# Performance work log

Hardware: AMD Instinct MI355X
Metric: run time of the kernel (lower is better)

The kernel has to match this reference:

```python
import jax, jax.numpy as jnp
import numpy as np

B, S, D, H = 2, 2048, 1024, 16  # batch, seq, embed_dim, num_heads
DH = D // H                      # head dim = 64


def setup_inputs() -> dict:
    key = jax.random.key(0)
    kx, kq, kbq, kk, kbk, kv, kbv = jax.random.split(key, 7)
    scale = 1.0 / np.sqrt(D)
    return {
        "x": jax.random.normal(kx, (B, S, D), dtype=jnp.float32),
        "Wq": jax.random.normal(kq, (D, D), dtype=jnp.float32) * scale,
        "bq": jax.random.normal(kbq, (D,), dtype=jnp.float32) * 0.01,
        "Wk": jax.random.normal(kk, (D, D), dtype=jnp.float32) * scale,
        "bk": jax.random.normal(kbk, (D,), dtype=jnp.float32) * 0.01,
        "Wv": jax.random.normal(kv, (D, D), dtype=jnp.float32) * scale,
        "bv": jax.random.normal(kbv, (D,), dtype=jnp.float32) * 0.01,
    }


def reference(x, Wq, bq, Wk, bk, Wv, bv):
    # ooqkv_type == 'q', odeint_method == 'id': q branch = act(Linear(x)), exact GELU (torch nn.GELU default)
    q = jax.nn.gelu(x @ Wq + bq, approximate=False)
    k = x @ Wk + bk
    v = x @ Wv + bv
    # [B, S, D] -> [B, S, H, DH]
    q = q.reshape(B, S, H, DH)
    k = k.reshape(B, S, H, DH)
    v = v.reshape(B, S, H, DH)
    # NOTE: original module has NO 1/sqrt(d) scale — faithful reproduction
    att = jnp.einsum("bqhd,bkhd->bhqk", q, k)
    att = jax.nn.softmax(att, axis=-1)
    out = jnp.einsum("bhqk,bkhd->bqhd", att, v)
    return out.reshape(B, S, D)
```

## Files before the change

### kernel.cpp

```cpp
#include <hip/hip_runtime.h>
#include <math.h>

#define B_  2
#define S_  2048
#define D_  1024
#define H_  16
#define DH_ 64
#define M_  (B_ * S_)

typedef _Float16 half_t;
typedef __attribute__((ext_vector_type(8))) _Float16 h8;
typedef __attribute__((ext_vector_type(4))) _Float16 h4;
typedef __attribute__((ext_vector_type(4))) float   f32x4;

#define LOG2E 1.44269504088896f

__device__ __forceinline__ void gll16(const half_t* g, half_t* l) {
    __builtin_amdgcn_global_load_lds(
        (__attribute__((address_space(1))) const void*)g,
        (__attribute__((address_space(3))) void*)l, 16, 0, 0);
}

__global__ __launch_bounds__(256) void prep_k(
    const float* __restrict__ x, half_t* __restrict__ xh,
    const float* __restrict__ Wq, const float* __restrict__ Wk,
    const float* __restrict__ Wv, half_t* __restrict__ Wt)
{
    const int bx = blockIdx.x;
    if (bx < 2048) {
        const size_t i = ((size_t)bx * 256 + threadIdx.x) * 8;
        const float4 a = *(const float4*)(x + i);
        const float4 b = *(const float4*)(x + i + 4);
        h8 o;
        o[0] = (half_t)a.x; o[1] = (half_t)a.y; o[2] = (half_t)a.z; o[3] = (half_t)a.w;
        o[4] = (half_t)b.x; o[5] = (half_t)b.y; o[6] = (half_t)b.z; o[7] = (half_t)b.w;
        *(h8*)(xh + i) = o;
    } else {
        const int gb    = bx - 2048;
        const int which = gb >> 9;
        const float* __restrict__ W = (which == 0) ? Wq : (which == 1) ? Wk : Wv;
        half_t* __restrict__ T = Wt + (size_t)which * D_ * D_;
        const int gw   = (gb & 511) * 4 + (threadIdx.x >> 6);
        const int lane = threadIdx.x & 63;
        const int n    = (gw & 15) * 64 + lane;
        const int k0   = (gw >> 4) * 8;
        h8 o;
        #pragma unroll
        for (int t = 0; t < 8; ++t) o[t] = (half_t)W[(size_t)(k0 + t) * D_ + n];
        *(h8*)(T + (size_t)n * D_ + k0) = o;
    }
}

__global__ __launch_bounds__(512) void qkv_gemm_f16(
    const half_t* __restrict__ xh, const half_t* __restrict__ Wt,
    const float* __restrict__ bq, const float* __restrict__ bk,
    const float* __restrict__ bv,
    half_t* __restrict__ Qo, half_t* __restrict__ Ko, half_t* __restrict__ Vt)
{
    const int lin = blockIdx.y * 24 + blockIdx.x;
    const int xcd = lin & 7;
    const int idx = lin >> 3;
    const int n0g = (xcd * 3 + idx % 3) * 128;
    const int m0  = (idx / 3) * 128;
    const int which = n0g >> 10;
    const int n0    = n0g & 1023;
    const half_t* __restrict__ Wp  = Wt + (size_t)which * D_ * D_;
    const float* __restrict__ bias = (which == 0) ? bq : (which == 1) ? bk : bv;

    const int tid = threadIdx.x, lane = tid & 63, wave = tid >> 6;
    const int wm = (wave & 3) * 32, wn = (wave >> 2) * 64;
    const int ln = lane & 15, quad = lane >> 4;

    __shared__ __align__(16) half_t SMEM[128 * 136];
    half_t* const As = SMEM;
    half_t* const Bs = SMEM + 128 * 64;

    const int r0  = tid >> 3, c0 = tid & 7;
    const int cs  = c0 ^ (r0 & 7);
    const half_t* aS = xh + (size_t)(m0 + r0) * D_ + cs * 8;
    const half_t* bS = Wp + (size_t)(n0 + r0) * D_ + cs * 8;

    f32x4 acc[2][4];
    #pragma unroll
    for (int i = 0; i < 2; ++i)
        #pragma unroll
        for (int j = 0; j < 4; ++j) acc[i][j] = (f32x4){0.f, 0.f, 0.f, 0.f};

    for (int k0 = 0; k0 < D_; k0 += 64) {
        __syncthreads();
        gll16(aS,            &As[tid * 8]);
        gll16(aS + 64 * D_,  &As[(tid + 512) * 8]);
        gll16(bS,            &Bs[tid * 8]);
        gll16(bS + 64 * D_,  &Bs[(tid + 512) * 8]);
        aS += 64; bS += 64;
        __syncthreads();

        #pragma unroll
        for (int kc = 0; kc < 2; ++kc) {
            h8 af[2], bf[4];
            #pragma unroll
            for (int i = 0; i < 2; ++i) {
                const int r = wm + i * 16 + ln;
                af[i] = *(const h8*)&As[r * 64 + (((kc << 2) + quad) ^ (r & 7)) * 8];
            }
            #pragma unroll
            for (int j = 0; j < 4; ++j) {
                const int r = wn + j * 16 + ln;
                bf[j] = *(const h8*)&Bs[r * 64 + (((kc << 2) + quad) ^ (r & 7)) * 8];
            }
            #pragma unroll
            for (int i = 0; i < 2; ++i)
                #pragma unroll
                for (int j = 0; j < 4; ++j)
                    acc[i][j] = __builtin_amdgcn_mfma_f32_16x16x32_f16(
                        af[i], bf[j], acc[i][j], 0, 0, 0);
        }
    }

    if (which == 2) {
        #pragma unroll
        for (int j = 0; j < 4; ++j) {
            const int col = n0 + wn + j * 16 + ln;
            const int h = col >> 6, d = col & 63;
            const float bb = bias[col];
            #pragma unroll
            for (int i = 0; i < 2; ++i) {
                const int sg = m0 + wm + i * 16 + quad * 4;
                const int b  = sg >> 11, srow = sg & 2047;
                h4 pv;
                #pragma unroll
                for (int r = 0; r < 4; ++r) pv[r] = (half_t)(acc[i][j][r] + bb);
                *(h4*)(Vt + (((size_t)(b * H_ + h) * DH_ + d) * S_ + srow)) = pv;
            }
        }
    } else {
        half_t* __restrict__ outp = (which == 0) ? Qo : Ko;
        __syncthreads();
        #pragma unroll
        for (int j = 0; j < 4; ++j) {
            const int col = wn + j * 16 + ln;
            const float bb = bias[n0 + col];
            #pragma unroll
            for (int i = 0; i < 2; ++i) {
                #pragma unroll
                for (int r = 0; r < 4; ++r) {
                    const int row = wm + i * 16 + quad * 4 + r;
                    float t = acc[i][j][r] + bb;
                    if (which == 0) {
                        const float u = t * fmaf(t * t, 0.0356774081f, 0.7978845608f);
                        const float e = __builtin_amdgcn_exp2f(u * -2.88539008178f);
                        t = t * __builtin_amdgcn_rcpf(1.0f + e) * LOG2E;
                    }
                    SMEM[row * 136 + col] = (half_t)t;
                }
            }
        }
        __syncthreads();
        const int cc = tid & 15;
        const int rr = tid >> 4;
        #pragma unroll
        for (int p = 0; p < 4; ++p) {
            const int row = p * 32 + rr;
            const h8 v = *(const h8*)&SMEM[row * 136 + cc * 8];
            *(h8*)(outp + (size_t)(m0 + row) * D_ + n0 + cc * 8) = v;
        }
    }
}

#define DEFER_THR 10.0f
#define ATTN_TILE(KS, VS)                                                     \
    do {                                                                      \
        f32x4 sa[4];                                                          \
        __builtin_amdgcn_s_setprio(1);                                        \
        _Pragma("unroll")                                                     \
        for (int j = 0; j < 4; ++j) {                                         \
            const int rK = j * 16 + ln;                                       \
            const h8 ka0 = *(const h8*)&KS[rK * 64 + ((quad)     ^ (rK & 7)) * 8]; \
            const h8 ka1 = *(const h8*)&KS[rK * 64 + ((quad + 4) ^ (rK & 7)) * 8]; \
            f32x4 t = (f32x4){0.f, 0.f, 0.f, 0.f};                            \
            t = __builtin_amdgcn_mfma_f32_16x16x32_f16(ka0, qa0, t, 0, 0, 0); \
            t = __builtin_amdgcn_mfma_f32_16x16x32_f16(ka1, qa1, t, 0, 0, 0); \
            sa[j] = t;                                                        \
        }                                                                     \
        __builtin_amdgcn_s_setprio(0);                                        \
        float mxa = sa[0][0];                                                 \
        _Pragma("unroll")                                                     \
        for (int j = 0; j < 4; ++j)                                           \
            _Pragma("unroll")                                                 \
            for (int r = 0; r < 4; ++r) mxa = fmaxf(mxa, sa[j][r]);           \
        mxa = fmaxf(mxa, __shfl_xor(mxa, 16, 64));                            \
        mxa = fmaxf(mxa, __shfl_xor(mxa, 32, 64));                            \
        if (__ballot(mxa > m_a + DEFER_THR)) {                                \
            const float mna = fmaxf(m_a, mxa);                                \
            const float ala = __builtin_amdgcn_exp2f(m_a - mna);              \
            m_a = mna;                                                        \
            float ra[4];                                                      \
            _Pragma("unroll")                                                 \
            for (int r = 0; r < 4; ++r) ra[r] = __shfl(ala, quad * 4 + r, 64);\
            _Pragma("unroll")                                                 \
            for (int r = 0; r < 4; ++r) {                                     \
                la[r] *= ra[r];                                               \
                _Pragma("unroll")                                             \
                for (int j = 0; j < 4; ++j) Oa[j][r] *= ra[r];                \
            }                                                                 \
        }                                                                     \
        _Pragma("unroll")                                                     \
        for (int j = 0; j < 4; ++j) {                                         \
            h4 pva;                                                           \
            _Pragma("unroll")                                                 \
            for (int r = 0; r < 4; ++r)                                       \
                pva[r] = (half_t)__builtin_amdgcn_exp2f(sa[j][r] - m_a);      \
            *(h4*)&QPs[wave * 16 + ln][j * 16 + quad * 4] = pva;              \
        }                                                                     \
        const h8 pa0 = *(const h8*)&QPs[wave * 16 + ln][quad * 8];            \
        const h8 pa1 = *(const h8*)&QPs[wave * 16 + ln][32 + quad * 8];       \
        __builtin_amdgcn_s_setprio(1);                                        \
        _Pragma("unroll")                                                     \
        for (int j = 0; j < 4; ++j) {                                         \
            const int rV = j * 16 + ln;                                       \
            const h8 vb0 = *(const h8*)&VS[rV * 64 + ((quad)     ^ (rV & 7)) * 8]; \
            const h8 vb1 = *(const h8*)&VS[rV * 64 + ((quad + 4) ^ (rV & 7)) * 8]; \
            Oa[j] = __builtin_amdgcn_mfma_f32_16x16x32_f16(pa0, vb0, Oa[j], 0, 0, 0); \
            Oa[j] = __builtin_amdgcn_mfma_f32_16x16x32_f16(pa1, vb1, Oa[j], 0, 0, 0); \
        }                                                                     \
        la = __builtin_amdgcn_mfma_f32_16x16x32_f16(pa0, ones8, la, 0, 0, 0); \
        la = __builtin_amdgcn_mfma_f32_16x16x32_f16(pa1, ones8, la, 0, 0, 0); \
        __builtin_amdgcn_s_setprio(0);                                        \
    } while (0)

__global__ __launch_bounds__(512) void attn_f16(
    const half_t* __restrict__ Q, const half_t* __restrict__ K,
    const half_t* __restrict__ Vt, float* __restrict__ out)
{
    const int tid  = threadIdx.x;
    const int lane = tid & 63;
    const int wave = tid >> 6;
    const int ln   = lane & 15;
    const int quad = lane >> 4;

    const int lin = blockIdx.y * 16 + blockIdx.x;
    const int swz = (lin & 7) * 64 + (lin >> 3);
    const int bh  = swz >> 4;
    const int b   = bh >> 4;
    const int h   = bh & 15;
    const int q0  = (swz & 15) * 128;

    const half_t* __restrict__ Qb  = Q  + (size_t)b * S_ * D_ + h * DH_;
    const half_t* __restrict__ Kb  = K  + (size_t)b * S_ * D_ + h * DH_;
    const half_t* __restrict__ Vtb = Vt + (size_t)bh * DH_ * S_;

    __shared__ __align__(16) half_t Ks0[64 * 64];
    __shared__ __align__(16) half_t Vs0[64 * 64];
    __shared__ __align__(16) half_t Ks1[64 * 64];
    __shared__ __align__(16) half_t Vs1[64 * 64];
    __shared__ __align__(16) half_t QPs[128][72];

    const int sr  = tid >> 3, sc0 = tid & 7;
    const int scs = sc0 ^ (sr & 7);
    const half_t* kS = Kb  + (size_t)sr * D_ + scs * 8;
    const half_t* vS = Vtb + (size_t)sr * S_ + scs * 8;
    half_t* const kD0 = &Ks0[tid * 8];
    half_t* const vD0 = &Vs0[tid * 8];
    half_t* const kD1 = &Ks1[tid * 8];
    half_t* const vD1 = &Vs1[tid * 8];

    gll16(kS, kD0); gll16(vS, vD0);
    kS += 64 * D_; vS += 64;

    #pragma unroll
    for (int l = 0; l < 2; ++l) {
        const int c = tid + l * 512;
        const int r = c >> 3, k8 = c & 7;
        *(h8*)&QPs[r][k8 * 8] = *(const h8*)(Qb + (size_t)(q0 + r) * D_ + k8 * 8);
    }
    __syncthreads();
    const h8 qa0 = *(const h8*)&QPs[wave * 16 + ln][quad * 8];
    const h8 qa1 = *(const h8*)&QPs[wave * 16 + ln][32 + quad * 8];

    h8 ones8;
    #pragma unroll
    for (int t = 0; t < 8; ++t) ones8[t] = (half_t)1.0f;

    f32x4 Oa[4];
    #pragma unroll
    for (int j = 0; j < 4; ++j) Oa[j] = (f32x4){0.f, 0.f, 0.f, 0.f};
    f32x4 la = (f32x4){0.f, 0.f, 0.f, 0.f};
    float m_a = -INFINITY;

    for (int it = 0; it < 16; ++it) {
        gll16(kS, kD1); gll16(vS, vD1);
        kS += 64 * D_; vS += 64;
        ATTN_TILE(Ks0, Vs0);
        __syncthreads();

        if (it < 15) {
            gll16(kS, kD0); gll16(vS, vD0);
            kS += 64 * D_; vS += 64;
        }
        ATTN_TILE(Ks1, Vs1);
        __syncthreads();
    }

    #pragma unroll
    for (int r = 0; r < 4; ++r) {
        const float iva = 1.0f / la[r];
        const int rowa = q0 + wave * 16 + quad * 4 + r;
        #pragma unroll
        for (int j = 0; j < 4; ++j)
            out[((size_t)b * S_ + rowa) * D_ + h * DH_ + j * 16 + ln] = Oa[j][r] * iva;
    }
}

extern "C" void kernel_launch(void* const* d_in, const int* in_sizes, int n_in,
                              void* d_out, int out_size, void* d_ws, size_t ws_size,
                              hipStream_t stream) {
    const float* x  = (const float*)d_in[0];
    const float* Wq = (const float*)d_in[1];
    const float* bq = (const float*)d_in[2];
    const float* Wk = (const float*)d_in[3];
    const float* bk = (const float*)d_in[4];
    const float* Wv = (const float*)d_in[5];
    const float* bv = (const float*)d_in[6];
    float* out = (float*)d_out;

    const size_t nmd = (size_t)M_ * D_;
    const size_t ndd = (size_t)D_ * D_;
    half_t* xh  = (half_t*)d_ws;
    half_t* Wt  = xh + nmd;
    half_t* Qh  = Wt + 3 * ndd;
    half_t* Kh  = Qh + nmd;
    half_t* Vtw = Kh + nmd;

    prep_k<<<2048 + 1536, 256, 0, stream>>>(x, xh, Wq, Wk, Wv, Wt);
    qkv_gemm_f16<<<dim3(3 * D_ / 128, M_ / 128), 512, 0, stream>>>(
        xh, Wt, bq, bk, bv, Qh, Kh, Vtw);
    attn_f16<<<dim3(S_ / 128, B_ * H_), 512, 0, stream>>>(Qh, Kh, Vtw, out);
}
```

Before: 168.3 us.

## Double-buffer QKV GEMM LDS tiles with BK=32 and tree-reduce attention row max

```diff
diff --git a/kernel.cpp b/kernel.cpp
--- a/kernel.cpp
+++ b/kernel.cpp
@@ -51,6 +51,32 @@
     }
 }
 
+#define QSLOT(r, q) \
+    (((((r) >> 1) * 8) + ((((((r) & 1) << 2) | (q))) ^ (((r) >> 1) & 7))) * 8)
+
+#define QKV_STEP(AS, BS)                                                      \
+    do {                                                                      \
+        h8 af[2], bf[4];                                                      \
+        _Pragma("unroll")                                                     \
+        for (int i = 0; i < 2; ++i) {                                         \
+            const int r = wm + i * 16 + ln;                                   \
+            af[i] = *(const h8*)&AS[QSLOT(r, quad)];                          \
+        }                                                                     \
+        _Pragma("unroll")                                                     \
+        for (int j = 0; j < 4; ++j) {                                         \
+            const int r = wn + j * 16 + ln;                                   \
+            bf[j] = *(const h8*)&BS[QSLOT(r, quad)];                          \
+        }                                                                     \
+        __builtin_amdgcn_s_setprio(1);                                        \
+        _Pragma("unroll")                                                     \
+        for (int i = 0; i < 2; ++i)                                           \
+            _Pragma("unroll")                                                 \
+            for (int j = 0; j < 4; ++j)                                       \
+                acc[i][j] = __builtin_amdgcn_mfma_f32_16x16x32_f16(           \
+                    af[i], bf[j], acc[i][j], 0, 0, 0);                        \
+        __builtin_amdgcn_s_setprio(0);                                        \
+    } while (0)
+
 __global__ __launch_bounds__(512) void qkv_gemm_f16(
     const half_t* __restrict__ xh, const half_t* __restrict__ Wt,
     const float* __restrict__ bq, const float* __restrict__ bk,
@@ -71,14 +97,17 @@
     const int wm = (wave & 3) * 32, wn = (wave >> 2) * 64;
     const int ln = lane & 15, quad = lane >> 4;
 
-    __shared__ __align__(16) half_t SMEM[128 * 136];
-    half_t* const As = SMEM;
-    half_t* const Bs = SMEM + 128 * 64;
-
-    const int r0  = tid >> 3, c0 = tid & 7;
-    const int cs  = c0 ^ (r0 & 7);
-    const half_t* aS = xh + (size_t)(m0 + r0) * D_ + cs * 8;
-    const half_t* bS = Wp + (size_t)(n0 + r0) * D_ + cs * 8;
+    __shared__ __align__(16) half_t As0[128 * 40];
+    __shared__ __align__(16) half_t Bs0[128 * 40];
+    __shared__ __align__(16) half_t As1[128 * 40];
+    __shared__ __align__(16) half_t Bs1[128 * 40];
+
+    const int srow = tid >> 3, sch = tid & 7;
+    const int v    = sch ^ (srow & 7);
+    const int sr   = srow * 2 + (v >> 2);
+    const int sk   = (v & 3) * 8;
+    const half_t* aS = xh + (size_t)(m0 + sr) * D_ + sk;
+    const half_t* bS = Wp + (size_t)(n0 + sr) * D_ + sk;
 
     f32x4 acc[2][4];
     #pragma unroll
@@ -86,35 +115,25 @@
         #pragma unroll
         for (int j = 0; j < 4; ++j) acc[i][j] = (f32x4){0.f, 0.f, 0.f, 0.f};
 
-    for (int k0 = 0; k0 < D_; k0 += 64) {
-        __syncthreads();
-        gll16(aS,            &As[tid * 8]);
-        gll16(aS + 64 * D_,  &As[(tid + 512) * 8]);
-        gll16(bS,            &Bs[tid * 8]);
-        gll16(bS + 64 * D_,  &Bs[(tid + 512) * 8]);
-        aS += 64; bS += 64;
-        __syncthreads();
-
-        #pragma unroll
-        for (int kc = 0; kc < 2; ++kc) {
-            h8 af[2], bf[4];
-            #pragma unroll
-            for (int i = 0; i < 2; ++i) {
-                const int r = wm + i * 16 + ln;
-                af[i] = *(const h8*)&As[r * 64 + (((kc << 2) + quad) ^ (r & 7)) * 8];
-            }
-            #pragma unroll
-            for (int j = 0; j < 4; ++j) {
-                const int r = wn + j * 16 + ln;
-                bf[j] = *(const h8*)&Bs[r * 64 + (((kc << 2) + quad) ^ (r & 7)) * 8];
-            }
-            #pragma unroll
-            for (int i = 0; i < 2; ++i)
-                #pragma unroll
-                for (int j = 0; j < 4; ++j)
-                    acc[i][j] = __builtin_amdgcn_mfma_f32_16x16x32_f16(
-                        af[i], bf[j], acc[i][j], 0, 0, 0);
-        }
+    gll16(aS, &As0[tid * 8]);
+    gll16(bS, &Bs0[tid * 8]);
+    aS += 32; bS += 32;
+    __syncthreads();
+
+    for (int it = 0; it < 16; ++it) {
+        gll16(aS, &As1[tid * 8]);
+        gll16(bS, &Bs1[tid * 8]);
+        aS += 32; bS += 32;
+        QKV_STEP(As0, Bs0);
+        __syncthreads();
+
+        if (it < 15) {
+            gll16(aS, &As0[tid * 8]);
+            gll16(bS, &Bs0[tid * 8]);
+            aS += 32; bS += 32;
+        }
+        QKV_STEP(As1, Bs1);
+        __syncthreads();
     }
 
     if (which == 2) {
@@ -126,20 +145,22 @@
             #pragma unroll
             for (int i = 0; i < 2; ++i) {
                 const int sg = m0 + wm + i * 16 + quad * 4;
-                const int b  = sg >> 11, srow = sg & 2047;
+                const int b  = sg >> 11, srw = sg & 2047;
                 h4 pv;
                 #pragma unroll
                 for (int r = 0; r < 4; ++r) pv[r] = (half_t)(acc[i][j][r] + bb);
-                *(h4*)(Vt + (((size_t)(b * H_ + h) * DH_ + d) * S_ + srow)) = pv;
+                *(h4*)(Vt + (((size_t)(b * H_ + h) * DH_ + d) * S_ + srw)) = pv;
             }
         }
     } else {
         half_t* __restrict__ outp = (which == 0) ? Qo : Ko;
-        __syncthreads();
         #pragma unroll
         for (int j = 0; j < 4; ++j) {
             const int col = wn + j * 16 + ln;
             const float bb = bias[n0 + col];
+            half_t* const pb = (wave & 4) ? ((j & 2) ? Bs1 : As1)
+                                          : ((j & 2) ? Bs0 : As0);
+            const int c32 = (j & 1) * 16 + ln;
             #pragma unroll
             for (int i = 0; i < 2; ++i) {
                 #pragma unroll
@@ -151,18 +172,21 @@
                         const float e = __builtin_amdgcn_exp2f(u * -2.88539008178f);
                         t = t * __builtin_amdgcn_rcpf(1.0f + e) * LOG2E;
                     }
-                    SMEM[row * 136 + col] = (half_t)t;
+                    pb[row * 40 + c32] = (half_t)t;
                 }
             }
         }
         __syncthreads();
         const int cc = tid & 15;
         const int rr = tid >> 4;
+        half_t* const pb = (cc & 8) ? ((cc & 4) ? Bs1 : As1)
+                                    : ((cc & 4) ? Bs0 : As0);
+        const int c32 = (cc & 3) * 8;
         #pragma unroll
         for (int p = 0; p < 4; ++p) {
             const int row = p * 32 + rr;
-            const h8 v = *(const h8*)&SMEM[row * 136 + cc * 8];
-            *(h8*)(outp + (size_t)(m0 + row) * D_ + n0 + cc * 8) = v;
+            const h8 vv = *(const h8*)&pb[row * 40 + c32];
+            *(h8*)(outp + (size_t)(m0 + row) * D_ + n0 + cc * 8) = vv;
         }
     }
 }
@@ -183,11 +207,12 @@
             sa[j] = t;                                                        \
         }                                                                     \
         __builtin_amdgcn_s_setprio(0);                                        \
-        float mxa = sa[0][0];                                                 \
+        float mj[4];                                                          \
         _Pragma("unroll")                                                     \
         for (int j = 0; j < 4; ++j)                                           \
-            _Pragma("unroll")                                                 \
-            for (int r = 0; r < 4; ++r) mxa = fmaxf(mxa, sa[j][r]);           \
+            mj[j] = fmaxf(fmaxf(sa[j][0], sa[j][1]),                          \
+                          fmaxf(sa[j][2], sa[j][3]));                         \
+        float mxa = fmaxf(fmaxf(mj[0], mj[1]), fmaxf(mj[2], mj[3]));          \
         mxa = fmaxf(mxa, __shfl_xor(mxa, 16, 64));                            \
         mxa = fmaxf(mxa, __shfl_xor(mxa, 32, 64));                            \
         if (__ballot(mxa > m_a + DEFER_THR)) {                                \
```

After: 176.6 us. +5.0%, slower.
